# Kernel tuning notes

Measured on AMD Instinct MI355X. Metric: run time of the kernel, lower is better.

## Reference

```python
import jax, jax.numpy as jnp
import numpy as np

B, C = 32, 32768
ENC_DIM, VOCAB, TOK_DIM, HIDDEN = 1024, 100000, 256, 512


def setup_inputs() -> dict:
    key = jax.random.key(0)
    k1, k2, k3, k4, k5 = jax.random.split(key, 5)
    enc_vec = jax.random.normal(k1, (B, ENC_DIM), dtype=jnp.float32)
    cand_tok = jax.random.randint(k2, (B, C), 0, VOCAB, dtype=jnp.int64)
    tok_emb = jax.random.normal(k3, (VOCAB, TOK_DIM), dtype=jnp.float32) * 0.02
    # PAD (0) and BOS (1) rows fixed to zeros, as in __init__
    tok_emb = tok_emb.at[0].set(0.0).at[1].set(0.0)
    W1 = jax.random.normal(k4, (HIDDEN, ENC_DIM), dtype=jnp.float32) * 0.02
    b1 = jnp.zeros((HIDDEN,), dtype=jnp.float32)
    W2 = jax.random.normal(k5, (TOK_DIM, HIDDEN), dtype=jnp.float32) * 0.02
    return {"enc_vec": enc_vec, "cand_tok": cand_tok, "tok_emb": tok_emb,
            "W1": W1, "b1": b1, "W2": W2}


def reference(enc_vec, cand_tok, tok_emb, W1, b1, W2):
    # q_proj: Linear -> GELU (exact, torch default) -> (Dropout inactive at eval) -> Linear (no bias)
    h = jax.nn.gelu(enc_vec @ W1.T + b1, approximate=False)  # (B, hidden)
    q = h @ W2.T                                             # (B, tok_dim)
    Wc = tok_emb[cand_tok]                                   # (B, C, tok_dim) gather
    logits = jnp.einsum('be,bce->bc', q, Wc)                 # (B, C)
    return logits
```

## Files before the change

kernel.cpp:

```cpp
#include <hip/hip_runtime.h>
#include <math.h>

#define B_    32
#define C_    32768
#define ENC_  1024
#define VOCAB_ 100000
#define TOK_  256
#define HID_  512

typedef __attribute__((ext_vector_type(8))) short short8;
typedef __attribute__((ext_vector_type(4))) float f32x4;

__device__ __forceinline__ float gelu_exact(float x) {
    return 0.5f * x * (1.0f + erff(x * 0.70710678118654752f));
}

__device__ __forceinline__ unsigned short f2bf(float f) {
    unsigned u = __builtin_bit_cast(unsigned, f);
    return (unsigned short)((u + 0x7fffu + ((u >> 16) & 1u)) >> 16);
}

__device__ __forceinline__ short8 pack8(float4 a, float4 b) {
    short8 r;
    r[0] = (short)f2bf(a.x); r[1] = (short)f2bf(a.y);
    r[2] = (short)f2bf(a.z); r[3] = (short)f2bf(a.w);
    r[4] = (short)f2bf(b.x); r[5] = (short)f2bf(b.y);
    r[6] = (short)f2bf(b.z); r[7] = (short)f2bf(b.w);
    return r;
}

__global__ __launch_bounds__(256) void k1_hidden(
    const float* __restrict__ enc, const float* __restrict__ W1,
    const float* __restrict__ b1, float* __restrict__ h)
{
    __shared__ float enc_lds[ENC_];
    const int b = blockIdx.y;
    const int tid = threadIdx.x;
    ((float4*)enc_lds)[tid] = ((const float4*)(enc + b * ENC_))[tid];
    __syncthreads();

    const int hw = tid >> 5, lane = tid & 31;
    const int jbase = blockIdx.x * 64 + hw * 8;
    const float4* enc4 = (const float4*)enc_lds;
    #pragma unroll
    for (int i = 0; i < 8; ++i) {
        const int j = jbase + i;
        const float4* wrow = (const float4*)(W1 + (size_t)j * ENC_);
        float acc = 0.f;
        #pragma unroll
        for (int t = 0; t < 8; ++t) {
            const int k4 = t * 32 + lane;
            float4 w = wrow[k4];
            float4 e = enc4[k4];
            acc += w.x * e.x + w.y * e.y + w.z * e.z + w.w * e.w;
        }
        #pragma unroll
        for (int m = 16; m >= 1; m >>= 1) acc += __shfl_xor(acc, m, 32);
        if (lane == 0) h[b * HID_ + j] = gelu_exact(acc + b1[j]);
    }
}

__global__ __launch_bounds__(256) void k2_q(
    const float* __restrict__ h, const float* __restrict__ W2,
    float* __restrict__ q)
{
    __shared__ float h_lds[HID_];
    const int b = blockIdx.y;
    const int tid = threadIdx.x;
    ((float2*)h_lds)[tid] = ((const float2*)(h + b * HID_))[tid];
    __syncthreads();

    const int hw = tid >> 5, lane = tid & 31;
    const int jbase = blockIdx.x * 64 + hw * 8;
    const float4* h4 = (const float4*)h_lds;
    #pragma unroll
    for (int i = 0; i < 8; ++i) {
        const int j = jbase + i;
        const float4* wrow = (const float4*)(W2 + (size_t)j * HID_);
        float acc = 0.f;
        #pragma unroll
        for (int t = 0; t < 4; ++t) {
            const int k4 = t * 32 + lane;
            float4 w = wrow[k4];
            float4 e = h4[k4];
            acc += w.x * e.x + w.y * e.y + w.z * e.z + w.w * e.w;
        }
        #pragma unroll
        for (int m = 16; m >= 1; m >>= 1) acc += __shfl_xor(acc, m, 32);
        if (lane == 0) q[b * TOK_ + j] = acc;
    }
}

__global__ __launch_bounds__(256) void k3_qall_mfma(
    const float* __restrict__ q, const float* __restrict__ tok_emb,
    float* __restrict__ q_allT)
{
    __shared__ short8 q_lds[1024];
    const int tid  = threadIdx.x;
    const int lane = tid & 63;
    const int hw   = tid >> 6;
    const int m  = lane & 15;
    const int kq = lane >> 4;

    #pragma unroll
    for (int ks2 = 0; ks2 < 2; ++ks2) {
        const int ks = hw * 2 + ks2;
        #pragma unroll
        for (int n = 0; n < 2; ++n) {
            const float4* p = (const float4*)(q + (n * 16 + m) * TOK_ + ks * 32 + kq * 8);
            q_lds[(ks * 2 + n) * 64 + lane] = pack8(p[0], p[1]);
        }
    }
    __syncthreads();

    const int wave = blockIdx.x * 4 + hw;
    if (wave >= VOCAB_ / 32) return;
    const int v0 = wave * 32;

    const float* abase = tok_emb + (size_t)(v0 + m) * TOK_ + kq * 8;

    float4 st[2][4];
    #pragma unroll
    for (int t = 0; t < 2; ++t) {
        st[0][t * 2 + 0] = *(const float4*)(abase + t * 16 * TOK_);
        st[0][t * 2 + 1] = *(const float4*)(abase + t * 16 * TOK_ + 4);
    }

    f32x4 acc[2][2] = {{{0.f,0.f,0.f,0.f},{0.f,0.f,0.f,0.f}},
                       {{0.f,0.f,0.f,0.f},{0.f,0.f,0.f,0.f}}};
    #pragma unroll
    for (int ks = 0; ks < 8; ++ks) {
        const int cur = ks & 1, nxt = cur ^ 1;
        if (ks < 7) {
            #pragma unroll
            for (int t = 0; t < 2; ++t) {
                st[nxt][t * 2 + 0] = *(const float4*)(abase + t * 16 * TOK_ + (ks + 1) * 32);
                st[nxt][t * 2 + 1] = *(const float4*)(abase + t * 16 * TOK_ + (ks + 1) * 32 + 4);
            }
        }
        short8 b0 = q_lds[(ks * 2 + 0) * 64 + lane];
        short8 b1 = q_lds[(ks * 2 + 1) * 64 + lane];
        #pragma unroll
        for (int t = 0; t < 2; ++t) {
            short8 af = pack8(st[cur][t * 2 + 0], st[cur][t * 2 + 1]);
            acc[t][0] = __builtin_amdgcn_mfma_f32_16x16x32_bf16(af, b0, acc[t][0], 0, 0, 0);
            acc[t][1] = __builtin_amdgcn_mfma_f32_16x16x32_bf16(af, b1, acc[t][1], 0, 0, 0);
        }
    }

    #pragma unroll
    for (int t = 0; t < 2; ++t) {
        #pragma unroll
        for (int i = 0; i < 4; ++i) {
            const int row = v0 + t * 16 + kq * 4 + i;
            float* dst = q_allT + (size_t)row * B_ + m;
            dst[0]  = acc[t][0][i];
            dst[16] = acc[t][1][i];
        }
    }
}

__global__ __launch_bounds__(256) void k4_gather(
    const int4* __restrict__ cand, const float* __restrict__ q_allT,
    float4* __restrict__ out)
{
    const int i = blockIdx.x * 256 + threadIdx.x;
    const int b = i >> 12;
    const int4 c0 = cand[i * 2];
    const int4 c1 = cand[i * 2 + 1];
    float4 r0, r1;
    r0.x = q_allT[(size_t)c0.x * B_ + b];
    r0.y = q_allT[(size_t)c0.y * B_ + b];
    r0.z = q_allT[(size_t)c0.z * B_ + b];
    r0.w = q_allT[(size_t)c0.w * B_ + b];
    r1.x = q_allT[(size_t)c1.x * B_ + b];
    r1.y = q_allT[(size_t)c1.y * B_ + b];
    r1.z = q_allT[(size_t)c1.z * B_ + b];
    r1.w = q_allT[(size_t)c1.w * B_ + b];
    out[i * 2]     = r0;
    out[i * 2 + 1] = r1;
}

extern "C" void kernel_launch(void* const* d_in, const int* in_sizes, int n_in,
                              void* d_out, int out_size, void* d_ws, size_t ws_size,
                              hipStream_t stream) {
    const float* enc     = (const float*)d_in[0];
    const int*   cand    = (const int*)  d_in[1];
    const float* tok_emb = (const float*)d_in[2];
    const float* W1      = (const float*)d_in[3];
    const float* b1      = (const float*)d_in[4];
    const float* W2      = (const float*)d_in[5];
    float* out = (float*)d_out;

    float* h      = (float*)d_ws;
    float* q      = h + B_ * HID_;
    float* q_allT = q + B_ * TOK_;

    k1_hidden<<<dim3(8, 32), 256, 0, stream>>>(enc, W1, b1, h);
    k2_q     <<<dim3(4, 32), 256, 0, stream>>>(h, W2, q);

    const int tiles = VOCAB_ / 32;
    k3_qall_mfma<<<(tiles + 3) / 4, 256, 0, stream>>>(q, tok_emb, q_allT);

    k4_gather<<<B_ * C_ / 2048, 256, 0, stream>>>((const int4*)cand, q_allT, (float4*)out);
}
```

Before: 205.0 us.

## Store projected vocab scores batch-major so gathers hit one contiguous row

```diff
diff --git a/kernel.cpp b/kernel.cpp
--- a/kernel.cpp
+++ b/kernel.cpp
@@ -93,7 +93,7 @@
 
 __global__ __launch_bounds__(256) void k3_qall_mfma(
     const float* __restrict__ q, const float* __restrict__ tok_emb,
-    float* __restrict__ q_allT)
+    float* __restrict__ q_all)
 {
     __shared__ short8 q_lds[1024];
     const int tid  = threadIdx.x;
@@ -151,34 +151,31 @@
     #pragma unroll
     for (int t = 0; t < 2; ++t) {
         #pragma unroll
-        for (int i = 0; i < 4; ++i) {
-            const int row = v0 + t * 16 + kq * 4 + i;
-            float* dst = q_allT + (size_t)row * B_ + m;
-            dst[0]  = acc[t][0][i];
-            dst[16] = acc[t][1][i];
+        for (int n = 0; n < 2; ++n) {
+            float4 r;
+            r.x = acc[t][n][0]; r.y = acc[t][n][1];
+            r.z = acc[t][n][2]; r.w = acc[t][n][3];
+            float* dst = q_all + (size_t)(n * 16 + m) * VOCAB_ + v0 + t * 16 + kq * 4;
+            *(float4*)dst = r;
         }
     }
 }
 
 __global__ __launch_bounds__(256) void k4_gather(
-    const int4* __restrict__ cand, const float* __restrict__ q_allT,
-    float4* __restrict__ out)
-{
-    const int i = blockIdx.x * 256 + threadIdx.x;
-    const int b = i >> 12;
-    const int4 c0 = cand[i * 2];
-    const int4 c1 = cand[i * 2 + 1];
-    float4 r0, r1;
-    r0.x = q_allT[(size_t)c0.x * B_ + b];
-    r0.y = q_allT[(size_t)c0.y * B_ + b];
-    r0.z = q_allT[(size_t)c0.z * B_ + b];
-    r0.w = q_allT[(size_t)c0.w * B_ + b];
-    r1.x = q_allT[(size_t)c1.x * B_ + b];
-    r1.y = q_allT[(size_t)c1.y * B_ + b];
-    r1.z = q_allT[(size_t)c1.z * B_ + b];
-    r1.w = q_allT[(size_t)c1.w * B_ + b];
-    out[i * 2]     = r0;
-    out[i * 2 + 1] = r1;
+    const int* __restrict__ cand, const float* __restrict__ q_all,
+    float* __restrict__ out)
+{
+    const int b     = blockIdx.x & 31;
+    const int chunk = blockIdx.x >> 5;
+    const int c0 = chunk * 1024 + threadIdx.x * 4;
+    const int4 t = *(const int4*)(cand + (size_t)b * C_ + c0);
+    const float* row = q_all + (size_t)b * VOCAB_;
+    float4 r;
+    r.x = row[t.x];
+    r.y = row[t.y];
+    r.z = row[t.z];
+    r.w = row[t.w];
+    *(float4*)(out + (size_t)b * C_ + c0) = r;
 }
 
 extern "C" void kernel_launch(void* const* d_in, const int* in_sizes, int n_in,
@@ -192,15 +189,15 @@
     const float* W2      = (const float*)d_in[5];
     float* out = (float*)d_out;
 
-    float* h      = (float*)d_ws;
-    float* q      = h + B_ * HID_;
-    float* q_allT = q + B_ * TOK_;
+    float* h     = (float*)d_ws;
+    float* q     = h + B_ * HID_;
+    float* q_all = q + B_ * TOK_;
 
     k1_hidden<<<dim3(8, 32), 256, 0, stream>>>(enc, W1, b1, h);
     k2_q     <<<dim3(4, 32), 256, 0, stream>>>(h, W2, q);
 
     const int tiles = VOCAB_ / 32;
-    k3_qall_mfma<<<(tiles + 3) / 4, 256, 0, stream>>>(q, tok_emb, q_allT);
-
-    k4_gather<<<B_ * C_ / 2048, 256, 0, stream>>>((const int4*)cand, q_allT, (float4*)out);
-}
+    k3_qall_mfma<<<(tiles + 3) / 4, 256, 0, stream>>>(q, tok_emb, q_all);
+
+    k4_gather<<<32 * 32, 256, 0, stream>>>(cand, q_all, out);
+}
```

Result: faster. 198.3 us (-3.3%).
